# Performance work log

Hardware: AMD Instinct MI355X
Metric: run time of the kernel (lower is better)

The kernel has to match this reference:

```python
import jax, jax.numpy as jnp
import numpy as np

N, E, F_IN, F_EXP, H, C = 8192, 65536, 3247, 7993, 3, 512
HC = H * C
NEG_SLOPE = 0.2


def setup_inputs() -> dict:
    key = jax.random.key(0)
    ks = jax.random.split(key, 40)
    s = 0.02
    rnd = lambda k, *sh: (jax.random.normal(k, sh, jnp.float32) * s)
    d = {}
    d['x'] = jax.random.normal(ks[0], (N, F_IN), jnp.float32)
    d['edge_index'] = jax.random.randint(ks[1], (2, E), 0, N, jnp.int32)
    d['exp'] = jax.random.normal(ks[2], (N, F_EXP), jnp.float32)
    # GATv2 layer 1 (in=3247)
    d['w1l'] = rnd(ks[3], F_IN, HC); d['b1l'] = rnd(ks[4], HC)
    d['w1r'] = rnd(ks[5], F_IN, HC); d['b1r'] = rnd(ks[6], HC)
    d['a1'] = rnd(ks[7], H, C);      d['o1'] = rnd(ks[8], HC)
    # GATv2 layer 2 (in=1536)
    d['w2l'] = rnd(ks[9], HC, HC);  d['b2l'] = rnd(ks[10], HC)
    d['w2r'] = rnd(ks[11], HC, HC); d['b2r'] = rnd(ks[12], HC)
    d['a2'] = rnd(ks[13], H, C);     d['o2'] = rnd(ks[14], HC)
    # GATv2 layer 3 (in=1536)
    d['w3l'] = rnd(ks[15], HC, HC); d['b3l'] = rnd(ks[16], HC)
    d['w3r'] = rnd(ks[17], HC, HC); d['b3r'] = rnd(ks[18], HC)
    d['a3'] = rnd(ks[19], H, C);     d['o3'] = rnd(ks[20], HC)
    # encoder: 7993 -> 4000 -> 1500 -> 512
    d['e1w'] = rnd(ks[21], F_EXP, 4000); d['e1b'] = rnd(ks[22], 4000)
    d['e2w'] = rnd(ks[23], 4000, 1500);  d['e2b'] = rnd(ks[24], 1500)
    d['e3w'] = rnd(ks[25], 1500, 512);   d['e3b'] = rnd(ks[26], 512)
    # head: 2048 -> 1024 -> 512 -> 1
    d['l1w'] = rnd(ks[27], HC + 512, 1024); d['l1b'] = rnd(ks[28], 1024)
    d['l2w'] = rnd(ks[29], 1024, 512);      d['l2b'] = rnd(ks[30], 512)
    d['l3w'] = rnd(ks[31], 512, 1);         d['l3b'] = rnd(ks[32], 1)
    return d


def gatv2(h, src, dst, wl, bl, wr, br, att, out_bias):
    # PyG GATv2Conv: e_ij = a^T LeakyReLU(W_l h_j + W_r h_i), softmax over j per target i,
    # out_i = sum_j alpha_ij * (W_l h_j), concat heads, + bias.
    xl = (h @ wl + bl).reshape(N, H, C)
    xr = (h @ wr + br).reshape(N, H, C)
    e = jax.nn.leaky_relu(xl[src] + xr[dst], NEG_SLOPE)      # [E', H, C]
    logit = jnp.einsum('ehc,hc->eh', e, att)                  # [E', H]
    m = jax.ops.segment_max(logit, dst, num_segments=N)       # [N, H]
    p = jnp.exp(logit - m[dst])
    z = jax.ops.segment_sum(p, dst, num_segments=N)
    alpha = p / z[dst]                                        # segment softmax
    out = jax.ops.segment_sum(alpha[:, :, None] * xl[src], dst, num_segments=N)
    return out.reshape(N, HC) + out_bias


def reference(x, edge_index, exp,
              w1l, b1l, w1r, b1r, a1, o1,
              w2l, b2l, w2r, b2r, a2, o2,
              w3l, b3l, w3r, b3r, a3, o3,
              e1w, e1b, e2w, e2b, e3w, e3b,
              l1w, l1b, l2w, l2b, l3w, l3b):
    loops = jnp.arange(N, dtype=edge_index.dtype)
    src = jnp.concatenate([edge_index[0], loops])  # add_self_loops=True (PyG default)
    dst = jnp.concatenate([edge_index[1], loops])
    h = jax.nn.relu(gatv2(x, src, dst, w1l, b1l, w1r, b1r, a1, o1))
    h = jax.nn.relu(gatv2(h, src, dst, w2l, b2l, w2r, b2r, a2, o2))
    h = jax.nn.relu(gatv2(h, src, dst, w3l, b3l, w3r, b3r, a3, o3))
    cell = jax.nn.relu(exp @ e1w + e1b)
    cell = jax.nn.relu(cell @ e2w + e2b)
    cell = cell @ e3w + e3b
    z = jnp.concatenate([h, cell], axis=1)  # [N, 2048]
    z = jax.nn.relu(z @ l1w + l1b)
    z = jax.nn.relu(z @ l2w + l2b)
    return z @ l3w + l3b  # [N, 1]
```

## Files before the change

### kernel.cpp

```cpp
#include <hip/hip_runtime.h>
#include <stdint.h>

#define NN 8192
#define NE 65536
#define ET (NE + NN)
#define F_IN   3247
#define F_IN_P 3264
#define F_EXP   7993
#define F_EXP_P 8000

typedef __attribute__((ext_vector_type(8))) short bf16x8;
typedef __attribute__((ext_vector_type(4))) float f32x4;

typedef const __attribute__((address_space(1))) void gvoid_t;
typedef __attribute__((address_space(3))) void lvoid_t;

__device__ __forceinline__ float bf2f(uint16_t u) {
  union { uint32_t i; float f; } v; v.i = ((uint32_t)u) << 16; return v.f;
}
__device__ __forceinline__ uint16_t f2bf(float f) {
  union { float f; uint32_t i; } v; v.f = f;
  uint32_t r = v.i + 0x7fffu + ((v.i >> 16) & 1u);
  return (uint16_t)(r >> 16);
}

__device__ __forceinline__ void gld_lds16(const void* g, void* l) {
  __builtin_amdgcn_global_load_lds((gvoid_t*)g, (lvoid_t*)l, 16, 0, 0);
}

#define SBAR() __builtin_amdgcn_sched_barrier(0)
#define BARRIER() do { SBAR(); __builtin_amdgcn_s_barrier(); SBAR(); } while (0)
#define VMCNT(n) asm volatile("s_waitcnt vmcnt(" #n ")" ::: "memory")
#define MFMA16(a, b, c) __builtin_amdgcn_mfma_f32_16x16x32_bf16(a, b, c, 0, 0, 0)

__device__ __forceinline__ void stage4(const char* src, char* dst, size_t Kb) {
#pragma unroll
  for (int j = 0; j < 4; ++j)
    gld_lds16(src + (size_t)(j * 64) * Kb, dst + j * 8192);
}

#define KTILE(T, BUF)                                                          \
  do {                                                                         \
    const char* aB_  = smem + (BUF) + arow;                                    \
    const char* bB_  = smem + 65536 + (BUF) + brow_o;                          \
    const char* aBn_ = smem + ((BUF) ^ 32768) + arow;                          \
    const bool nls = ((T) + 2 < nk);                                           \
    const bool nlr = ((T) + 1 < nk);                                           \
                        \
    if (nlr) { VMCNT(8); } else { VMCNT(0); }                                  \
    _Pragma("unroll")                                                          \
    for (int n = 0; n < 2; ++n) {                                              \
      b01[n * 2]     = *(const bf16x8*)(bB_ + n * 2048 + sw0);                 \
      b01[n * 2 + 1] = *(const bf16x8*)(bB_ + n * 2048 + sw1);                 \
    }                                                                          \
    _Pragma("unroll")                                                          \
    for (int n = 0; n < 2; ++n) {                                              \
      b23[n * 2]     = *(const bf16x8*)(bB_ + (n + 2) * 2048 + sw0);           \
      b23[n * 2 + 1] = *(const bf16x8*)(bB_ + (n + 2) * 2048 + sw1);           \
    }                                                                          \
    SBAR();                                                                    \
    __builtin_amdgcn_s_setprio(1);                                             \
    _Pragma("unroll")                                                          \
    for (int m = 0; m < 4; ++m)                                                \
      _Pragma("unroll")                                                        \
      for (int n = 0; n < 2; ++n) {                                            \
        acc[m][n] = MFMA16(a03[m * 2],     b01[n * 2],     acc[m][n]);         \
        acc[m][n] = MFMA16(a03[m * 2 + 1], b01[n * 2 + 1], acc[m][n]);         \
      }                                                                        \
    __builtin_amdgcn_s_setprio(0);                                             \
    BARRIER();                                                                 \
                                        \
    _Pragma("unroll")                                                          \
    for (int m = 0; m < 4; ++m) {                                              \
      a47[m * 2]     = *(const bf16x8*)(aB_ + (m + 4) * 2048 + sw0);           \
      a47[m * 2 + 1] = *(const bf16x8*)(aB_ + (m + 4) * 2048 + sw1);           \
    }                                                                          \
    SBAR();                                                                    \
    __builtin_amdgcn_s_setprio(1);                                             \
    _Pragma("unroll")                                                          \
    for (int m = 0; m < 4; ++m)                                                \
      _Pragma("unroll")                                                        \
      for (int n = 0; n < 2; ++n) {                                            \
        acc[m][n + 2] = MFMA16(a03[m * 2],     b23[n * 2],     acc[m][n + 2]); \
        acc[m][n + 2] = MFMA16(a03[m * 2 + 1], b23[n * 2 + 1], acc[m][n + 2]); \
      }                                                                        \
    __builtin_amdgcn_s_setprio(0);                                             \
    BARRIER();                                                                 \
                       \
    if (nls) stage4(pA + (size_t)((T) + 2) * 128, sA + (BUF), Kb);             \
    _Pragma("unroll")                                                          \
    for (int n = 0; n < 2; ++n) {                                              \
      b01[n * 2]     = *(const bf16x8*)(bB_ + n * 2048 + sw0);                 \
      b01[n * 2 + 1] = *(const bf16x8*)(bB_ + n * 2048 + sw1);                 \
    }                                                                          \
    SBAR();                                                                    \
    __builtin_amdgcn_s_setprio(1);                                             \
    _Pragma("unroll")                                                          \
    for (int m = 0; m < 4; ++m)                                                \
      _Pragma("unroll")                                                        \
      for (int n = 0; n < 2; ++n) {                                            \
        acc[m + 4][n + 2] = MFMA16(a47[m * 2],     b23[n * 2],     acc[m + 4][n + 2]); \
        acc[m + 4][n + 2] = MFMA16(a47[m * 2 + 1], b23[n * 2 + 1], acc[m + 4][n + 2]); \
      }                                                                        \
    __builtin_amdgcn_s_setprio(0);                                             \
    BARRIER();                                                                 \
       \
    if (nls)      { VMCNT(8); }                                                \
    else if (nlr) { VMCNT(4); }                                                \
    if (nlr) {                                                                 \
      _Pragma("unroll")                                                        \
      for (int m = 0; m < 4; ++m) {                                            \
        a03[m * 2]     = *(const bf16x8*)(aBn_ + m * 2048 + sw0);              \
        a03[m * 2 + 1] = *(const bf16x8*)(aBn_ + m * 2048 + sw1);              \
      }                                                                        \
    }                                                                          \
    if (nls) stage4(pB + (size_t)((T) + 2) * 128, sB + (BUF), Kb);             \
    SBAR();                                                                    \
    __builtin_amdgcn_s_setprio(1);                                             \
    _Pragma("unroll")                                                          \
    for (int m = 0; m < 4; ++m)                                                \
      _Pragma("unroll")                                                        \
      for (int n = 0; n < 2; ++n) {                                            \
        acc[m + 4][n] = MFMA16(a47[m * 2],     b01[n * 2],     acc[m + 4][n]); \
        acc[m + 4][n] = MFMA16(a47[m * 2 + 1], b01[n * 2 + 1], acc[m + 4][n]); \
      }                                                                        \
    __builtin_amdgcn_s_setprio(0);                                             \
    BARRIER();                                                                 \
  } while (0)

__global__ __launch_bounds__(512, 2)
void gemm256(const uint16_t* __restrict__ A, const uint16_t* __restrict__ Bt,
             const float* __restrict__ bias, int biasN, int relu,
             uint16_t* __restrict__ C, int Kp, int ldc, int nbn)
{
  extern __shared__ char smem[];
  const int tid = threadIdx.x;
  const int w = tid >> 6, lane = tid & 63;
  const int wr = w >> 2, wc = w & 3;
  const int fr = lane & 15, g = lane >> 4;

  const int nwg = (int)gridDim.x;
  const int id = (int)blockIdx.x;
  const int q = nwg >> 3, r = nwg & 7;
  const int xcd = id & 7, idx = id >> 3;
  const int wg = (xcd < r ? xcd * (q + 1) : r * (q + 1) + (xcd - r) * q) + idx;
  const int brow = (wg / nbn) * 256, bcol = (wg % nbn) * 256;

  const size_t Kb = (size_t)Kp * 2;

  const int srow = tid >> 3;
  const int sswz = ((tid & 7) ^ (srow & 7)) * 16;
  const char* pA = (const char*)A + (size_t)(brow + srow) * Kb + sswz;
  const char* pB = (const char*)Bt + (size_t)(bcol + srow) * Kb + sswz;
  char* sA = smem + w * 1024;
  char* sB = smem + 65536 + w * 1024;

  const int sw0 = (g ^ (fr & 7)) * 16;
  const int sw1 = ((g + 4) ^ (fr & 7)) * 16;
  const int arow = (wr * 128 + fr) * 128;
  const int brow_o = (wc * 64 + fr) * 128;

  f32x4 acc[8][4];
#pragma unroll
  for (int m = 0; m < 8; ++m)
#pragma unroll
    for (int n = 0; n < 4; ++n) acc[m][n] = (f32x4){0.f, 0.f, 0.f, 0.f};
  bf16x8 a03[8], a47[8], b01[4], b23[4];

  stage4(pA, sA, Kb);
  stage4(pB, sB, Kb);
  stage4(pA + 128, sA + 32768, Kb);
  stage4(pB + 128, sB + 32768, Kb);
  VMCNT(8);
  BARRIER();
  {
    const char* aB = smem + arow;
#pragma unroll
    for (int m = 0; m < 4; ++m) {
      a03[m * 2]     = *(const bf16x8*)(aB + m * 2048 + sw0);
      a03[m * 2 + 1] = *(const bf16x8*)(aB + m * 2048 + sw1);
    }
  }
  SBAR();

  const int nk = Kp >> 6;
  for (int t = 0; t < nk; t += 2) {
    KTILE(t, 0);
    if (t + 1 < nk) KTILE(t + 1, 32768);
  }

#pragma unroll
  for (int m = 0; m < 8; ++m) {
    const int row = brow + wr * 128 + m * 16 + g * 4;
#pragma unroll
    for (int n = 0; n < 4; ++n) {
      const int col = bcol + wc * 64 + n * 16 + fr;
      const float bv = (col < biasN) ? bias[col] : 0.f;
#pragma unroll
      for (int j = 0; j < 4; ++j) {
        float v = acc[m][n][j] + bv;
        if (relu) v = fmaxf(v, 0.f);
        C[(size_t)(row + j) * ldc + col] = f2bf(v);
      }
    }
  }
}

__global__ __launch_bounds__(256)
void gemm_bt(const uint16_t* __restrict__ A, const uint16_t* __restrict__ Bt,
             const float* __restrict__ bias, int biasN, int relu,
             uint16_t* __restrict__ C, int Kp, int ldc)
{
  __shared__ uint16_t As[128 * 32];
  __shared__ uint16_t Bs[128 * 32];
  const int tid  = threadIdx.x;
  const int wave = tid >> 6, lane = tid & 63;
  const int brow = blockIdx.x * 128, bcol = blockIdx.y * 128;
  const int wr = wave >> 1, wc = wave & 1;
  const int fr = lane & 15, g = lane >> 4;

  f32x4 acc[4][4];
#pragma unroll
  for (int m = 0; m < 4; ++m)
#pragma unroll
    for (int n = 0; n < 4; ++n) acc[m][n] = (f32x4){0.f, 0.f, 0.f, 0.f};

  const int rA = tid >> 2;
  const int kc = (tid & 3) * 8;
  const uint16_t* aptr = A  + (size_t)(brow + rA) * Kp + kc;
  const uint16_t* bptr = Bt + (size_t)(bcol + rA) * Kp + kc;
  char* ldsA = (char*)As + wave * 1024;
  char* ldsB = (char*)Bs + wave * 1024;
  const size_t rowskip = (size_t)64 * Kp;

  const int nk = Kp >> 5;
  for (int kt = 0; kt < nk; ++kt) {
    __syncthreads();
    gld_lds16(aptr,           ldsA);
    gld_lds16(aptr + rowskip, ldsA + 4096);
    gld_lds16(bptr,           ldsB);
    gld_lds16(bptr + rowskip, ldsB + 4096);
    aptr += 32; bptr += 32;
    __syncthreads();

    bf16x8 af[4], bfr[4];
#pragma unroll
    for (int m = 0; m < 4; ++m)
      af[m] = *(const bf16x8*)&As[(wr * 64 + m * 16 + fr) * 32 + g * 8];
#pragma unroll
    for (int n = 0; n < 4; ++n)
      bfr[n] = *(const bf16x8*)&Bs[(wc * 64 + n * 16 + fr) * 32 + g * 8];
#pragma unroll
    for (int m = 0; m < 4; ++m)
#pragma unroll
      for (int n = 0; n < 4; ++n)
        acc[m][n] = MFMA16(af[m], bfr[n], acc[m][n]);
  }

#pragma unroll
  for (int m = 0; m < 4; ++m) {
    const int row = brow + wr * 64 + m * 16 + g * 4;
#pragma unroll
    for (int n = 0; n < 4; ++n) {
      const int col = bcol + wc * 64 + n * 16 + fr;
      const float bv = (col < biasN) ? bias[col] : 0.f;
#pragma unroll
      for (int j = 0; j < 4; ++j) {
        float v = acc[m][n][j] + bv;
        if (relu) v = fmaxf(v, 0.f);
        C[(size_t)(row + j) * ldc + col] = f2bf(v);
      }
    }
  }
}

__global__ __launch_bounds__(256)
void cvt_pad(const float* __restrict__ in, uint16_t* __restrict__ out, int cols, int colsPad)
{
  const int r = blockIdx.y;
  const int c = (blockIdx.x * 256 + threadIdx.x) * 2;
  if (c >= colsPad) return;
  const float* ip = in + (size_t)r * cols;
  const float v0 = (c < cols)     ? ip[c]     : 0.f;
  const float v1 = (c + 1 < cols) ? ip[c + 1] : 0.f;
  const uint32_t pk = (uint32_t)f2bf(v0) | ((uint32_t)f2bf(v1) << 16);
  *(uint32_t*)(out + (size_t)r * colsPad + c) = pk;
}

__global__ __launch_bounds__(256)
void transpose_w(const float* __restrict__ W, uint16_t* __restrict__ Wt,
                 int K, int N, int Kp, int Np)
{
  __shared__ float t[32][33];
  const int tx = threadIdx.x, ty = threadIdx.y;
  const int k0 = blockIdx.x * 32, n0 = blockIdx.y * 32;
#pragma unroll
  for (int j = 0; j < 4; ++j) {
    const int k = k0 + ty + j * 8, n = n0 + tx;
    t[ty + j * 8][tx] = (k < K && n < N) ? W[(size_t)k * N + n] : 0.f;
  }
  __syncthreads();
#pragma unroll
  for (int j = 0; j < 4; ++j) {
    const int n = n0 + ty + j * 8, k = k0 + tx;
    Wt[(size_t)n * Kp + k] = f2bf(t[tx][ty + j * 8]);
  }
}

__global__ void concat_bias(const float* __restrict__ bl, const float* __restrict__ br,
                            float* __restrict__ out)
{
  const int i = blockIdx.x * 256 + threadIdx.x;
  if (i < 1536) out[i] = bl[i];
  else if (i < 3072) out[i] = br[i - 1536];
}

__global__ void count_deg(const int* __restrict__ ei, int* __restrict__ counts)
{
  const int e = blockIdx.x * 256 + threadIdx.x;
  if (e >= ET) return;
  const int d = (e < NE) ? ei[NE + e] : (e - NE);
  atomicAdd(&counts[d], 1);
}

__global__ __launch_bounds__(1024)
void scan_deg(const int* __restrict__ counts, int* __restrict__ row_start, int* __restrict__ cursor)
{
  __shared__ int part[1024];
  const int tid = threadIdx.x;
  int loc[8], pre[8], s = 0;
#pragma unroll
  for (int j = 0; j < 8; ++j) { loc[j] = counts[tid * 8 + j]; pre[j] = s; s += loc[j]; }
  part[tid] = s;
  __syncthreads();
  for (int o = 1; o < 1024; o <<= 1) {
    const int v = part[tid];
    const int a = (tid >= o) ? part[tid - o] : 0;
    __syncthreads();
    part[tid] = v + a;
    __syncthreads();
  }
  const int excl = part[tid] - s;
#pragma unroll
  for (int j = 0; j < 8; ++j) {
    const int v = excl + pre[j];
    row_start[tid * 8 + j] = v;
    cursor[tid * 8 + j]    = v;
  }
  if (tid == 1023) row_start[8192] = excl + s;
}

__global__ void scatter_e(const int* __restrict__ ei, int* __restrict__ cursor,
                          int* __restrict__ csr_src, int* __restrict__ csr_dst)
{
  const int e = blockIdx.x * 256 + threadIdx.x;
  if (e >= ET) return;
  const int sx = (e < NE) ? ei[e]      : (e - NE);
  const int d  = (e < NE) ? ei[NE + e] : (e - NE);
  const int pos = atomicAdd(&cursor[d], 1);
  csr_src[pos] = sx;
  csr_dst[pos] = d;
}

__global__ __launch_bounds__(256)
void gat_fused(const uint16_t* __restrict__ xlr, int ld,
               const int* __restrict__ csr_src, const int* __restrict__ row_start,
               const float* __restrict__ att, const float* __restrict__ ob,
               uint16_t* __restrict__ out, int ldc)
{
  const int node = (blockIdx.x << 2) + (threadIdx.x >> 6);
  const int lane = threadIdx.x & 63;

  float av[3][8], xr[3][8];
  const bf16x8* pr = (const bf16x8*)(xlr + (size_t)node * ld + 1536);
#pragma unroll
  for (int h = 0; h < 3; ++h) {
    const float4 a0 = *(const float4*)(att + h * 512 + lane * 8);
    const float4 a1 = *(const float4*)(att + h * 512 + lane * 8 + 4);
    av[h][0] = a0.x; av[h][1] = a0.y; av[h][2] = a0.z; av[h][3] = a0.w;
    av[h][4] = a1.x; av[h][5] = a1.y; av[h][6] = a1.z; av[h][7] = a1.w;
    const bf16x8 v = pr[h * 64 + lane];
#pragma unroll
    for (int j = 0; j < 8; ++j) xr[h][j] = bf2f((uint16_t)v[j]);
  }

  float m[3] = {-1e30f, -1e30f, -1e30f};
  float z[3] = {0.f, 0.f, 0.f};
  float acc[3][8];
#pragma unroll
  for (int h = 0; h < 3; ++h)
#pragma unroll
    for (int j = 0; j < 8; ++j) acc[h][j] = 0.f;

  const int s0 = row_start[node], s1 = row_start[node + 1];
  for (int s = s0; s < s1; ++s) {
    const bf16x8* pl = (const bf16x8*)(xlr + (size_t)csr_src[s] * ld);
    bf16x8 vl[3];
#pragma unroll
    for (int h = 0; h < 3; ++h) vl[h] = pl[h * 64 + lane];

    float hacc[3];
#pragma unroll
    for (int h = 0; h < 3; ++h) {
      float sacc = 0.f;
#pragma unroll
      for (int j = 0; j < 8; ++j) {
        float v = bf2f((uint16_t)vl[h][j]) + xr[h][j];
        v = v > 0.f ? v : 0.2f * v;
        sacc += v * av[h][j];
      }
      hacc[h] = sacc;
    }
#pragma unroll
    for (int o = 32; o; o >>= 1) {
      hacc[0] += __shfl_xor(hacc[0], o);
      hacc[1] += __shfl_xor(hacc[1], o);
      hacc[2] += __shfl_xor(hacc[2], o);
    }
#pragma unroll
    for (int h = 0; h < 3; ++h) {
      const float nm = fmaxf(m[h], hacc[h]);
      const float sc = __expf(m[h] - nm);
      const float p  = __expf(hacc[h] - nm);
      z[h] = z[h] * sc + p;
#pragma unroll
      for (int j = 0; j < 8; ++j)
        acc[h][j] = acc[h][j] * sc + p * bf2f((uint16_t)vl[h][j]);
      m[h] = nm;
    }
  }

#pragma unroll
  for (int h = 0; h < 3; ++h) {
    const float rz = 1.f / z[h];
    const float4 b0 = *(const float4*)(ob + h * 512 + lane * 8);
    const float4 b1 = *(const float4*)(ob + h * 512 + lane * 8 + 4);
    float bv[8] = {b0.x, b0.y, b0.z, b0.w, b1.x, b1.y, b1.z, b1.w};
    bf16x8 pk;
#pragma unroll
    for (int j = 0; j < 8; ++j) {
      const float v = fmaxf(acc[h][j] * rz + bv[j], 0.f);
      pk[j] = (short)f2bf(v);
    }
    *(bf16x8*)(out + (size_t)node * ldc + h * 512 + lane * 8) = pk;
  }
}

__global__ __launch_bounds__(256)
void final_dot(const uint16_t* __restrict__ z2, const float* __restrict__ w,
               const float* __restrict__ b, float* __restrict__ out)
{
  const int row  = blockIdx.x * 4 + (threadIdx.x >> 6);
  const int lane = threadIdx.x & 63;
  const uint16_t* p = z2 + (size_t)row * 512;
  float s = 0.f;
#pragma unroll
  for (int j = 0; j < 8; ++j) { const int c = lane + j * 64; s += bf2f(p[c]) * w[c]; }
#pragma unroll
  for (int o = 32; o; o >>= 1) s += __shfl_xor(s, o);
  if (lane == 0) out[row] = s + b[0];
}

extern "C" void kernel_launch(void* const* d_in, const int* in_sizes, int n_in,
                              void* d_out, int out_size, void* d_ws, size_t ws_size,
                              hipStream_t stream)
{
  (void)in_sizes; (void)n_in; (void)out_size; (void)ws_size;

  const float* x    = (const float*)d_in[0];
  const int*   ei   = (const int*)  d_in[1];
  const float* expm = (const float*)d_in[2];
  const float* w1l = (const float*)d_in[3];  const float* b1l = (const float*)d_in[4];
  const float* w1r = (const float*)d_in[5];  const float* b1r = (const float*)d_in[6];
  const float* a1  = (const float*)d_in[7];  const float* o1  = (const float*)d_in[8];
  const float* w2l = (const float*)d_in[9];  const float* b2l = (const float*)d_in[10];
  const float* w2r = (const float*)d_in[11]; const float* b2r = (const float*)d_in[12];
  const float* a2  = (const float*)d_in[13]; const float* o2  = (const float*)d_in[14];
  const float* w3l = (const float*)d_in[15]; const float* b3l = (const float*)d_in[16];
  const float* w3r = (const float*)d_in[17]; const float* b3r = (const float*)d_in[18];
  const float* a3  = (const float*)d_in[19]; const float* o3  = (const float*)d_in[20];
  const float* e1w = (const float*)d_in[21]; const float* e1b = (const float*)d_in[22];
  const float* e2w = (const float*)d_in[23]; const float* e2b = (const float*)d_in[24];
  const float* e3w = (const float*)d_in[25]; const float* e3b = (const float*)d_in[26];
  const float* l1w = (const float*)d_in[27]; const float* l1b = (const float*)d_in[28];
  const float* l2w = (const float*)d_in[29]; const float* l2b = (const float*)d_in[30];
  const float* l3w = (const float*)d_in[31]; const float* l3b = (const float*)d_in[32];
  float* out = (float*)d_out;

  hipFuncSetAttribute((const void*)gemm256, hipFuncAttributeMaxDynamicSharedMemorySize, 131072);

  char* ws = (char*)d_ws;
  size_t off = 0;
  auto take = [&](size_t b) { char* p = ws + off; off += (b + 255) & ~(size_t)255; return p; };

  int*      counts    = (int*)take((size_t)NN * 4);
  int*      row_start = (int*)take((size_t)(NN + 1) * 4);
  int*      cursor    = (int*)take((size_t)NN * 4);
  int*      csr_src   = (int*)take((size_t)ET * 4);
  int*      csr_dst   = (int*)take((size_t)ET * 4);
  float*    bc1       = (float*)take(3072 * 4);
  float*    bc2       = (float*)take(3072 * 4);
  float*    bc3       = (float*)take(3072 * 4);
  uint16_t* zbuf      = (uint16_t*)take((size_t)NN * 2048 * 2);
  char*     regA      = take((size_t)NN * F_EXP_P * 2);
  char*     regW      = take((size_t)4096 * F_EXP_P * 2);
  char*     regC      = take((size_t)NN * 4096 * 2 + (size_t)NN * 1536 * 2);

  uint16_t* xbf   = (uint16_t*)regA;
  uint16_t* expbf = (uint16_t*)regA;
  uint16_t* wT    = (uint16_t*)regW;
  uint16_t* xlr   = (uint16_t*)regC;
  uint16_t* hbuf  = (uint16_t*)(regC + (size_t)NN * 3072 * 2);
  uint16_t* cell1 = (uint16_t*)regC;
  uint16_t* cell2 = (uint16_t*)(regC + (size_t)NN * 4096 * 2);
  uint16_t* zz1   = (uint16_t*)regC;
  uint16_t* zz2   = (uint16_t*)(regC + (size_t)NN * 1024 * 2);

  hipMemsetAsync(counts, 0, (size_t)NN * 4, stream);
  count_deg<<<(ET + 255) / 256, 256, 0, stream>>>(ei, counts);
  scan_deg<<<1, 1024, 0, stream>>>(counts, row_start, cursor);
  scatter_e<<<(ET + 255) / 256, 256, 0, stream>>>(ei, cursor, csr_src, csr_dst);
  concat_bias<<<12, 256, 0, stream>>>(b1l, b1r, bc1);
  concat_bias<<<12, 256, 0, stream>>>(b2l, b2r, bc2);
  concat_bias<<<12, 256, 0, stream>>>(b3l, b3r, bc3);

  cvt_pad<<<dim3((F_IN_P / 2 + 255) / 256, NN), 256, 0, stream>>>(x, xbf, F_IN, F_IN_P);
  transpose_w<<<dim3(F_IN_P / 32, 1536 / 32), dim3(32, 8), 0, stream>>>(w1l, wT, F_IN, 1536, F_IN_P, 1536);
  transpose_w<<<dim3(F_IN_P / 32, 1536 / 32), dim3(32, 8), 0, stream>>>(w1r, wT + (size_t)1536 * F_IN_P, F_IN, 1536, F_IN_P, 1536);
  gemm256<<<32 * 12, 512, 131072, stream>>>(xbf, wT, bc1, 3072, 0, xlr, F_IN_P, 3072, 12);
  gat_fused<<<NN / 4, 256, 0, stream>>>(xlr, 3072, csr_src, row_start, a1, o1, hbuf, 1536);

  transpose_w<<<dim3(48, 48), dim3(32, 8), 0, stream>>>(w2l, wT, 1536, 1536, 1536, 1536);
  transpose_w<<<dim3(48, 48), dim3(32, 8), 0, stream>>>(w2r, wT + (size_t)1536 * 1536, 1536, 1536, 1536, 1536);
  gemm256<<<32 * 12, 512, 131072, stream>>>(hbuf, wT, bc2, 3072, 0, xlr, 1536, 3072, 12);
  gat_fused<<<NN / 4, 256, 0, stream>>>(xlr, 3072, csr_src, row_start, a2, o2, hbuf, 1536);

  transpose_w<<<dim3(48, 48), dim3(32, 8), 0, stream>>>(w3l, wT, 1536, 1536, 1536, 1536);
  transpose_w<<<dim3(48, 48), dim3(32, 8), 0, stream>>>(w3r, wT + (size_t)1536 * 1536, 1536, 1536, 1536, 1536);
  gemm256<<<32 * 12, 512, 131072, stream>>>(hbuf, wT, bc3, 3072, 0, xlr, 1536, 3072, 12);
  gat_fused<<<NN / 4, 256, 0, stream>>>(xlr, 3072, csr_src, row_start, a3, o3, zbuf, 2048);

  cvt_pad<<<dim3((F_EXP_P / 2 + 255) / 256, NN), 256, 0, stream>>>(expm, expbf, F_EXP, F_EXP_P);
  transpose_w<<<dim3(F_EXP_P / 32, 4096 / 32), dim3(32, 8), 0, stream>>>(e1w, wT, F_EXP, 4000, F_EXP_P, 4096);
  gemm256<<<32 * 16, 512, 131072, stream>>>(expbf, wT, e1b, 4000, 1, cell1, F_EXP_P, 4096, 16);
  transpose_w<<<dim3(4096 / 32, 1536 / 32), dim3(32, 8), 0, stream>>>(e2w, wT, 4000, 1500, 4096, 1536);
  gemm256<<<32 * 6, 512, 131072, stream>>>(cell1, wT, e2b, 1500, 1, cell2, 4096, 1536, 6);
  transpose_w<<<dim3(1536 / 32, 512 / 32), dim3(32, 8), 0, stream>>>(e3w, wT, 1500, 512, 1536, 512);
  gemm_bt<<<dim3(64, 4), 256, 0, stream>>>(cell2, wT, e3b, 512, 0, zbuf + 1536, 1536, 2048);

  transpose_w<<<dim3(2048 / 32, 1024 / 32), dim3(32, 8), 0, stream>>>(l1w, wT, 2048, 1024, 2048, 1024);
  gemm_bt<<<dim3(64, 8), 256, 0, stream>>>(zbuf, wT, l1b, 1024, 1, zz1, 2048, 1024);
  transpose_w<<<dim3(1024 / 32, 512 / 32), dim3(32, 8), 0, stream>>>(l2w, wT, 1024, 512, 1024, 512);
  gemm_bt<<<dim3(64, 4), 256, 0, stream>>>(zz1, wT, l2b, 512, 1, zz2, 1024, 512);
  final_dot<<<NN / 4, 256, 0, stream>>>(zz2, l3w, l3b, out);
}
```

Before: 1.468 ms.

## Spread GEMM global-to-LDS prefetches across MFMA phases with finer vmcnt waits

Replaces the two 4-load staging bursts per K-tile with four 2-load bursts, each issued inside a different MFMA phase. B for the next tile is now loaded one step ahead instead of two, while A stays two tiles ahead. The s_waitcnt points move to just before the barriers. The goal is to smooth memory issue and overlap it better with MFMA work, at the cost of a shorter prefetch distance for B, which could expose latency.

Result: slower. 1.699 ms (+15.8%).

```diff
diff --git a/kernel.cpp b/kernel.cpp
--- a/kernel.cpp
+++ b/kernel.cpp
@@ -33,10 +33,9 @@
 #define VMCNT(n) asm volatile("s_waitcnt vmcnt(" #n ")" ::: "memory")
 #define MFMA16(a, b, c) __builtin_amdgcn_mfma_f32_16x16x32_bf16(a, b, c, 0, 0, 0)
 
-__device__ __forceinline__ void stage4(const char* src, char* dst, size_t Kb) {
-#pragma unroll
-  for (int j = 0; j < 4; ++j)
-    gld_lds16(src + (size_t)(j * 64) * Kb, dst + j * 8192);
+__device__ __forceinline__ void stage2(const char* src, char* dst, size_t Kb) {
+  gld_lds16(src, dst);
+  gld_lds16(src + (size_t)64 * Kb, dst + 8192);
 }
 
 #define KTILE(T, BUF)                                                          \
@@ -44,10 +43,11 @@
     const char* aB_  = smem + (BUF) + arow;                                    \
     const char* bB_  = smem + 65536 + (BUF) + brow_o;                          \
     const char* aBn_ = smem + ((BUF) ^ 32768) + arow;                          \
+    char* sAt = sA + (BUF);                                                    \
+    char* sBo = sB + ((BUF) ^ 32768);                                          \
     const bool nls = ((T) + 2 < nk);                                           \
     const bool nlr = ((T) + 1 < nk);                                           \
-                        \
-    if (nlr) { VMCNT(8); } else { VMCNT(0); }                                  \
+             \
     _Pragma("unroll")                                                          \
     for (int n = 0; n < 2; ++n) {                                              \
       b01[n * 2]     = *(const bf16x8*)(bB_ + n * 2048 + sw0);                 \
@@ -58,6 +58,7 @@
       b23[n * 2]     = *(const bf16x8*)(bB_ + (n + 2) * 2048 + sw0);           \
       b23[n * 2 + 1] = *(const bf16x8*)(bB_ + (n + 2) * 2048 + sw1);           \
     }                                                                          \
+    if (nlr) stage2(pB + (size_t)((T) + 1) * 128, sBo, Kb);                    \
     SBAR();                                                                    \
     __builtin_amdgcn_s_setprio(1);                                             \
     _Pragma("unroll")                                                          \
@@ -69,12 +70,13 @@
       }                                                                        \
     __builtin_amdgcn_s_setprio(0);                                             \
     BARRIER();                                                                 \
-                                        \
+                 \
     _Pragma("unroll")                                                          \
     for (int m = 0; m < 4; ++m) {                                              \
       a47[m * 2]     = *(const bf16x8*)(aB_ + (m + 4) * 2048 + sw0);           \
       a47[m * 2 + 1] = *(const bf16x8*)(aB_ + (m + 4) * 2048 + sw1);           \
     }                                                                          \
+    if (nlr) stage2(pB + (size_t)((T) + 1) * 128 + 128 * Kb, sBo + 16384, Kb); \
     SBAR();                                                                    \
     __builtin_amdgcn_s_setprio(1);                                             \
     _Pragma("unroll")                                                          \
@@ -86,13 +88,13 @@
       }                                                                        \
     __builtin_amdgcn_s_setprio(0);                                             \
     BARRIER();                                                                 \
-                       \
-    if (nls) stage4(pA + (size_t)((T) + 2) * 128, sA + (BUF), Kb);             \
+     \
     _Pragma("unroll")                                                          \
     for (int n = 0; n < 2; ++n) {                                              \
       b01[n * 2]     = *(const bf16x8*)(bB_ + n * 2048 + sw0);                 \
       b01[n * 2 + 1] = *(const bf16x8*)(bB_ + n * 2048 + sw1);                 \
     }                                                                          \
+    if (nls) stage2(pA + (size_t)((T) + 2) * 128, sAt, Kb);                    \
     SBAR();                                                                    \
     __builtin_amdgcn_s_setprio(1);                                             \
     _Pragma("unroll")                                                          \
@@ -103,10 +105,9 @@
         acc[m + 4][n + 2] = MFMA16(a47[m * 2 + 1], b23[n * 2 + 1], acc[m + 4][n + 2]); \
       }                                                                        \
     __builtin_amdgcn_s_setprio(0);                                             \
+    if (nlr) { if (nls) { VMCNT(6); } else { VMCNT(4); } }                     \
     BARRIER();                                                                 \
-       \
-    if (nls)      { VMCNT(8); }                                                \
-    else if (nlr) { VMCNT(4); }                                                \
+     \
     if (nlr) {                                                                 \
       _Pragma("unroll")                                                        \
       for (int m = 0; m < 4; ++m) {                                            \
@@ -114,7 +115,7 @@
         a03[m * 2 + 1] = *(const bf16x8*)(aBn_ + m * 2048 + sw1);              \
       }                                                                        \
     }                                                                          \
-    if (nls) stage4(pB + (size_t)((T) + 2) * 128, sB + (BUF), Kb);             \
+    if (nls) stage2(pA + (size_t)((T) + 2) * 128 + 128 * Kb, sAt + 16384, Kb); \
     SBAR();                                                                    \
     __builtin_amdgcn_s_setprio(1);                                             \
     _Pragma("unroll")                                                          \
@@ -125,6 +126,7 @@
         acc[m + 4][n] = MFMA16(a47[m * 2 + 1], b01[n * 2 + 1], acc[m + 4][n]); \
       }                                                                        \
     __builtin_amdgcn_s_setprio(0);                                             \
+    if (nlr) { if (nls) { VMCNT(4); } else { VMCNT(0); } }                     \
     BARRIER();                                                                 \
   } while (0)
 
@@ -167,11 +169,13 @@
     for (int n = 0; n < 4; ++n) acc[m][n] = (f32x4){0.f, 0.f, 0.f, 0.f};
   bf16x8 a03[8], a47[8], b01[4], b23[4];
 
-  stage4(pA, sA, Kb);
-  stage4(pB, sB, Kb);
-  stage4(pA + 128, sA + 32768, Kb);
-  stage4(pB + 128, sB + 32768, Kb);
-  VMCNT(8);
+  stage2(pA, sA, Kb);
+  stage2(pA + 128 * Kb, sA + 16384, Kb);
+  stage2(pB, sB, Kb);
+  stage2(pB + 128 * Kb, sB + 16384, Kb);
+  stage2(pA + 128, sA + 32768, Kb);
+  stage2(pA + 128 + 128 * Kb, sA + 32768 + 16384, Kb);
+  VMCNT(4);
   BARRIER();
   {
     const char* aB = smem + arow;
```
